# Kernel tuning notes

Hardware: AMD Instinct MI355X
Metric: run time of the kernel (lower is better)

Reference implementation:

```python
import jax, jax.numpy as jnp
import numpy as np

N_NODES = 50000
N_EDGES = 1600000
D_FEAT = 512
FILTERS = 256
NUM_CLASSES = 16


def setup_inputs() -> dict:
    key = jax.random.key(0)
    k = jax.random.split(key, 6)
    x = jax.random.normal(k[0], (N_NODES, D_FEAT), dtype=jnp.float32)
    W1 = jax.random.normal(k[1], (D_FEAT, FILTERS), dtype=jnp.float32) * (1.0 / np.sqrt(D_FEAT))
    W2 = jax.random.normal(k[2], (FILTERS, NUM_CLASSES), dtype=jnp.float32) * (1.0 / np.sqrt(FILTERS))
    edge_weight = jax.random.uniform(k[3], (N_EDGES,), dtype=jnp.float32)
    edge_src = jax.random.randint(k[4], (N_EDGES,), 0, N_NODES, dtype=jnp.int32)
    edge_dst = jax.random.randint(k[5], (N_EDGES,), 0, N_NODES, dtype=jnp.int32)
    return {"x": x, "W1": W1, "W2": W2, "edge_weight": edge_weight,
            "edge_src": edge_src, "edge_dst": edge_dst}


def _propagate(h, edge_src, edge_dst, edge_weight):
    # sparse A @ h: out[dst] += w * h[src]
    msgs = edge_weight[:, None] * h[edge_src]          # [E, F]
    return jax.ops.segment_sum(msgs, edge_dst, num_segments=N_NODES)


def reference(x, W1, W2, edge_weight, edge_src, edge_dst):
    # Dropout layers are identity at inference (training=False).
    # Layer 1: relu(A @ (X @ W1))
    h = jax.nn.relu(_propagate(x @ W1, edge_src, edge_dst, edge_weight))
    # Layer 2: softmax(A @ (H @ W2))
    logits = _propagate(h @ W2, edge_src, edge_dst, edge_weight)
    return jax.nn.softmax(logits, axis=-1)
```

## Files before the change

### kernel.cpp

```cpp
#include <hip/hip_runtime.h>

#define N_NODES 50000
#define N_EDGES 1600000
#define D_FEAT 512
#define FILTERS 256
#define NUM_CLASSES 16

typedef __bf16 bf16x8 __attribute__((ext_vector_type(8)));
typedef float f32x4 __attribute__((ext_vector_type(4)));
typedef _Float16 half4 __attribute__((ext_vector_type(4)));
typedef _Float16 f16x8 __attribute__((ext_vector_type(8)));

#define GLOAD_LDS16(g, l)                                                  \
  __builtin_amdgcn_global_load_lds(                                        \
      (const __attribute__((address_space(1))) unsigned int*)(g),          \
      (__attribute__((address_space(3))) unsigned int*)(l), 16, 0, 0)

__global__ __launch_bounds__(256) void split_w1_kernel(
    const float* __restrict__ W1, __bf16* __restrict__ Wth,
    __bf16* __restrict__ Wtl) {
  const int idx = blockIdx.x * 256 + threadIdx.x;
  const int k = idx >> 8;
  const int n = idx & 255;
  const float v = W1[idx];
  const __bf16 h = (__bf16)v;
  const __bf16 l = (__bf16)(v - (float)h);
  Wth[n * D_FEAT + k] = h;
  Wtl[n * D_FEAT + k] = l;
}

__global__ __launch_bounds__(256) void gemm1_mfma_kernel(
    const float* __restrict__ A, const __bf16* __restrict__ Bh,
    const __bf16* __restrict__ Bl, _Float16* __restrict__ C) {
  const int K = D_FEAT;
  __shared__ __bf16 sAh[128 * 32];
  __shared__ __bf16 sAl[128 * 32];
  __shared__ __bf16 sBh[128 * 32];
  __shared__ __bf16 sBl[128 * 32];

  const int tid = threadIdx.x;
  const int wave = tid >> 6;
  const int lane = tid & 63;
  const int wm = (wave >> 1) * 64;
  const int wn = (wave & 1) * 64;
  const int m0 = blockIdx.x * 128;
  const int n0 = blockIdx.y * 128;

  const int arow = tid >> 1;
  const int aks = (tid & 1) * 16;
  int am = m0 + arow;
  if (am >= N_NODES) am = N_NODES - 1;
  const float* aptr = A + (size_t)am * K + aks;

  const int lr = lane >> 2;
  const int lc = (lane & 3) * 8;
  const int fm = lane & 15;
  const int fq = lane >> 4;

  f32x4 acc[4][4] = {};

  for (int k0 = 0; k0 < K; k0 += 32) {
    const float4* ap = (const float4*)(aptr + k0);
    const float4 a0 = ap[0], a1 = ap[1], a2 = ap[2], a3 = ap[3];

    __syncthreads();

#pragma unroll
    for (int i = 0; i < 2; ++i) {
      const int row = wave * 32 + i * 16;
      GLOAD_LDS16(Bh + (size_t)(n0 + row + lr) * K + k0 + lc, sBh + row * 32);
      GLOAD_LDS16(Bl + (size_t)(n0 + row + lr) * K + k0 + lc, sBl + row * 32);
    }

    float va[16] = {a0.x, a0.y, a0.z, a0.w, a1.x, a1.y, a1.z, a1.w,
                    a2.x, a2.y, a2.z, a2.w, a3.x, a3.y, a3.z, a3.w};
    __bf16 hh[16], ll[16];
#pragma unroll
    for (int i = 0; i < 16; ++i) {
      const __bf16 h = (__bf16)va[i];
      hh[i] = h;
      ll[i] = (__bf16)(va[i] - (float)h);
    }
    *(bf16x8*)(sAh + arow * 32 + aks) = *(bf16x8*)&hh[0];
    *(bf16x8*)(sAh + arow * 32 + aks + 8) = *(bf16x8*)&hh[8];
    *(bf16x8*)(sAl + arow * 32 + aks) = *(bf16x8*)&ll[0];
    *(bf16x8*)(sAl + arow * 32 + aks + 8) = *(bf16x8*)&ll[8];

    __syncthreads();

    bf16x8 fah[4], fal[4], fbh[4], fbl[4];
#pragma unroll
    for (int t = 0; t < 4; ++t) {
      const int moff = (wm + t * 16 + fm) * 32 + fq * 8;
      fah[t] = *(const bf16x8*)(sAh + moff);
      fal[t] = *(const bf16x8*)(sAl + moff);
      const int noff = (wn + t * 16 + fm) * 32 + fq * 8;
      fbh[t] = *(const bf16x8*)(sBh + noff);
      fbl[t] = *(const bf16x8*)(sBl + noff);
    }
#pragma unroll
    for (int i = 0; i < 4; ++i)
#pragma unroll
      for (int j = 0; j < 4; ++j)
        acc[i][j] = __builtin_amdgcn_mfma_f32_16x16x32_bf16(fah[i], fbh[j],
                                                            acc[i][j], 0, 0, 0);
#pragma unroll
    for (int i = 0; i < 4; ++i)
#pragma unroll
      for (int j = 0; j < 4; ++j)
        acc[i][j] = __builtin_amdgcn_mfma_f32_16x16x32_bf16(fah[i], fbl[j],
                                                            acc[i][j], 0, 0, 0);
#pragma unroll
    for (int i = 0; i < 4; ++i)
#pragma unroll
      for (int j = 0; j < 4; ++j)
        acc[i][j] = __builtin_amdgcn_mfma_f32_16x16x32_bf16(fal[i], fbh[j],
                                                            acc[i][j], 0, 0, 0);
  }

#pragma unroll
  for (int ti = 0; ti < 4; ++ti) {
#pragma unroll
    for (int r = 0; r < 4; ++r) {
      const int m = m0 + wm + ti * 16 + fq * 4 + r;
      if (m < N_NODES) {
#pragma unroll
        for (int tj = 0; tj < 4; ++tj) {
          const int n = n0 + wn + tj * 16 + fm;
          C[(size_t)m * FILTERS + n] = (_Float16)acc[ti][tj][r];
        }
      }
    }
  }
}

__global__ __launch_bounds__(256) void hist_kernel(const int* __restrict__ edst,
                                                   int* __restrict__ deg) {
  const int e = blockIdx.x * 256 + threadIdx.x;
  if (e < N_EDGES) atomicAdd(&deg[edst[e]], 1);
}

#define SCAN_NB 196
__global__ __launch_bounds__(256) void scan_blocks_kernel(
    const int* __restrict__ deg, int* __restrict__ row_ptr,
    int* __restrict__ bsum) {
  __shared__ int s[256];
  const int i = blockIdx.x * 256 + threadIdx.x;
  const int v = (i < N_NODES) ? deg[i] : 0;
  s[threadIdx.x] = v;
  __syncthreads();
  for (int off = 1; off < 256; off <<= 1) {
    const int t = (threadIdx.x >= off) ? s[threadIdx.x - off] : 0;
    __syncthreads();
    s[threadIdx.x] += t;
    __syncthreads();
  }
  if (i < N_NODES) row_ptr[i] = s[threadIdx.x] - v;
  if (threadIdx.x == 255) bsum[blockIdx.x] = s[255];
}

__global__ __launch_bounds__(256) void scan_sums_kernel(int* __restrict__ bsum) {
  __shared__ int s[256];
  const int v = (threadIdx.x < SCAN_NB) ? bsum[threadIdx.x] : 0;
  s[threadIdx.x] = v;
  __syncthreads();
  for (int off = 1; off < 256; off <<= 1) {
    const int t = (threadIdx.x >= off) ? s[threadIdx.x - off] : 0;
    __syncthreads();
    s[threadIdx.x] += t;
    __syncthreads();
  }
  if (threadIdx.x < SCAN_NB) bsum[threadIdx.x] = s[threadIdx.x] - v;
}

__global__ __launch_bounds__(256) void scan_add_kernel(
    int* __restrict__ row_ptr, const int* __restrict__ bsum,
    int* __restrict__ cursor) {
  const int i = blockIdx.x * 256 + threadIdx.x;
  if (i < N_NODES) {
    const int r = row_ptr[i] + bsum[blockIdx.x];
    row_ptr[i] = r;
    cursor[i] = r;
  }
  if (i == 0) row_ptr[N_NODES] = N_EDGES;
}

__global__ __launch_bounds__(256) void fill_kernel(
    const int* __restrict__ esrc, const int* __restrict__ edst,
    const float* __restrict__ ew, int* __restrict__ cursor,
    int4* __restrict__ meta) {
  const int e = blockIdx.x * 256 + threadIdx.x;
  if (e >= N_EDGES) return;
  const int d = edst[e];
  const int pos = atomicAdd(&cursor[d], 1);
  meta[pos] = make_int4(esrc[e], __float_as_int(ew[e]), d, 0);
}

__global__ __launch_bounds__(256) void gather1_gemm2_kernel(
    const _Float16* __restrict__ xw1, const int* __restrict__ row_ptr,
    const int4* __restrict__ meta, const float* __restrict__ W2,
    _Float16* __restrict__ h2) {
  __shared__ float red[4][16][17];
  const int wave = threadIdx.x >> 6;
  const int lane = threadIdx.x & 63;
  const int node = blockIdx.x * 4 + wave;
  const int beg = row_ptr[node];
  const int end = row_ptr[node + 1];

  float acc[4] = {};
  const half4* __restrict__ xw1v = (const half4*)xw1;

  for (int c0 = beg; c0 < end; c0 += 64) {
    const int cnt = min(64, end - c0);
    const int4 mv = meta[c0 + ((lane < cnt) ? lane : 0)];

    for (int j = 0; j < cnt; j += 8) {
      int srcs[8];
      float ws[8];
#pragma unroll
      for (int u = 0; u < 8; ++u) {
        const int live = (j + u < cnt);
        const int l = live ? (j + u) : 0;
        srcs[u] = __builtin_amdgcn_readlane(mv.x, l);
        const int wb = __builtin_amdgcn_readlane(mv.y, l);
        ws[u] = live ? __int_as_float(wb) : 0.f;
      }
      half4 v[8];
#pragma unroll
      for (int u = 0; u < 8; ++u)
        v[u] = xw1v[(unsigned)srcs[u] * 64u + (unsigned)lane];
#pragma unroll
      for (int u = 0; u < 8; ++u)
#pragma unroll
        for (int i = 0; i < 4; ++i)
          acc[i] = fmaf(ws[u], (float)v[u][i], acc[i]);
    }
  }

  float r[4];
#pragma unroll
  for (int i = 0; i < 4; ++i) r[i] = fmaxf(acc[i], 0.f);

  float p[16] = {};
#pragma unroll
  for (int j = 0; j < 4; ++j) {
    const float4* wr = (const float4*)(W2 + (size_t)(lane * 4 + j) * NUM_CLASSES);
#pragma unroll
    for (int c4 = 0; c4 < 4; ++c4) {
      const float4 wv = wr[c4];
      p[c4 * 4 + 0] = fmaf(r[j], wv.x, p[c4 * 4 + 0]);
      p[c4 * 4 + 1] = fmaf(r[j], wv.y, p[c4 * 4 + 1]);
      p[c4 * 4 + 2] = fmaf(r[j], wv.z, p[c4 * 4 + 2]);
      p[c4 * 4 + 3] = fmaf(r[j], wv.w, p[c4 * 4 + 3]);
    }
  }

#pragma unroll
  for (int off = 32; off >= 16; off >>= 1)
#pragma unroll
    for (int i = 0; i < 16; ++i) p[i] += __shfl_xor(p[i], off, 64);

  if (lane < 16) {
#pragma unroll
    for (int i = 0; i < 16; ++i) red[wave][lane][i] = p[i];
  }
  if (lane < 16) {
    float sum = 0.f;
#pragma unroll
    for (int i = 0; i < 16; ++i) sum += red[wave][i][lane];
    h2[(size_t)node * NUM_CLASSES + lane] = (_Float16)sum;
  }
}

__global__ __launch_bounds__(256) void gather2_mfma_kernel(
    const _Float16* __restrict__ h2, const int* __restrict__ row_ptr,
    const int4* __restrict__ meta, float* __restrict__ out) {
  __shared__ _Float16 lds[4][16][72];
  const int wave = threadIdx.x >> 6;
  const int lane = threadIdx.x & 63;
  const int tile = blockIdx.x * 4 + wave;
  if (tile >= N_NODES / 16) return;
  const int t0 = tile * 16;
  const int beg = row_ptr[t0];
  const int end = row_ptr[t0 + 16];

  const int cls = lane & 15;
  const int kq = lane >> 4;
  const int erow = lane >> 1;
  const int part = lane & 1;

  f32x4 acc = {0.f, 0.f, 0.f, 0.f};
  _Float16* myl = &lds[wave][0][0];

  if (beg < end) {
    const int last = end - 1;
    int e = beg + lane;
    int4 m = meta[(e <= last) ? e : last];
    float wv = (e <= last) ? __int_as_float(m.y) : 0.f;

    for (int c0 = beg; c0 < end; c0 += 64) {
      int4 mn = m;
      float wn = 0.f;
      const int c1 = c0 + 64;
      if (c1 < end) {
        const int en = c1 + lane;
        mn = meta[(en <= last) ? en : last];
        wn = (en <= last) ? __int_as_float(mn.y) : 0.f;
      }

      const int se0 = __shfl(m.x, erow, 64);
      const int se1 = __shfl(m.x, 32 + erow, 64);
      const f16x8 r0 =
          *(const f16x8*)(h2 + (size_t)se0 * NUM_CLASSES + part * 8);
      const f16x8 r1 =
          *(const f16x8*)(h2 + (size_t)se1 * NUM_CLASSES + part * 8);

      f16x8 a0, a1;
#pragma unroll
      for (int j = 0; j < 8; ++j) {
        const int ei = kq * 8 + j;
        const int d0 = __shfl(m.z, ei, 64) - t0;
        const float w0 = __shfl(wv, ei, 64);
        a0[j] = (d0 == cls) ? (_Float16)w0 : (_Float16)0.f;
        const int d1 = __shfl(m.z, 32 + ei, 64) - t0;
        const float w1 = __shfl(wv, 32 + ei, 64);
        a1[j] = (d1 == cls) ? (_Float16)w1 : (_Float16)0.f;
      }

#pragma unroll
      for (int j = 0; j < 8; ++j) myl[(part * 8 + j) * 72 + erow] = r0[j];
#pragma unroll
      for (int j = 0; j < 8; ++j) myl[(part * 8 + j) * 72 + 32 + erow] = r1[j];

      const f16x8 b0 = *(const f16x8*)(myl + cls * 72 + kq * 8);
      const f16x8 b1 = *(const f16x8*)(myl + cls * 72 + 32 + kq * 8);

      acc = __builtin_amdgcn_mfma_f32_16x16x32_f16(a0, b0, acc, 0, 0, 0);
      acc = __builtin_amdgcn_mfma_f32_16x16x32_f16(a1, b1, acc, 0, 0, 0);

      m = mn;
      wv = wn;
    }
  }

#pragma unroll
  for (int r = 0; r < 4; ++r) {
    const float a = acc[r];
    float mx = a;
#pragma unroll
    for (int off = 8; off >= 1; off >>= 1)
      mx = fmaxf(mx, __shfl_xor(mx, off, 16));
    const float ex = __expf(a - mx);
    float sm = ex;
#pragma unroll
    for (int off = 8; off >= 1; off >>= 1) sm += __shfl_xor(sm, off, 16);
    out[(size_t)(t0 + kq * 4 + r) * NUM_CLASSES + cls] = ex / sm;
  }
}

extern "C" void kernel_launch(void* const* d_in, const int* in_sizes, int n_in,
                              void* d_out, int out_size, void* d_ws,
                              size_t ws_size, hipStream_t stream) {
  const float* x = (const float*)d_in[0];
  const float* W1 = (const float*)d_in[1];
  const float* W2 = (const float*)d_in[2];
  const float* ew = (const float*)d_in[3];
  const int* esrc = (const int*)d_in[4];
  const int* edst = (const int*)d_in[5];
  float* out = (float*)d_out;

  _Float16* xw1 = (_Float16*)d_ws;
  _Float16* h2 = xw1 + (size_t)N_NODES * FILTERS;
  int* row_ptr = (int*)(h2 + (size_t)N_NODES * NUM_CLASSES);
  int* cursor = row_ptr + (N_NODES + 1);
  int* deg = cursor + N_NODES;
  int4* meta = (int4*)(((uintptr_t)(deg + N_NODES) + 15) & ~(uintptr_t)15);
  __bf16* w1th = (__bf16*)(meta + N_EDGES);
  __bf16* w1tl = w1th + D_FEAT * FILTERS;
  int* bsum = (int*)(w1tl + D_FEAT * FILTERS);

  hipMemsetAsync(deg, 0, N_NODES * sizeof(int), stream);
  hist_kernel<<<(N_EDGES + 255) / 256, 256, 0, stream>>>(edst, deg);
  scan_blocks_kernel<<<SCAN_NB, 256, 0, stream>>>(deg, row_ptr, bsum);
  scan_sums_kernel<<<1, 256, 0, stream>>>(bsum);
  scan_add_kernel<<<SCAN_NB, 256, 0, stream>>>(row_ptr, bsum, cursor);
  fill_kernel<<<(N_EDGES + 255) / 256, 256, 0, stream>>>(esrc, edst, ew,
                                                         cursor, meta);

  split_w1_kernel<<<(D_FEAT * FILTERS) / 256, 256, 0, stream>>>(W1, w1th, w1tl);
  dim3 g1((N_NODES + 127) / 128, FILTERS / 128);
  gemm1_mfma_kernel<<<g1, 256, 0, stream>>>(x, w1th, w1tl, xw1);

  gather1_gemm2_kernel<<<N_NODES / 4, 256, 0, stream>>>(xw1, row_ptr, meta, W2,
                                                        h2);

  gather2_mfma_kernel<<<(N_NODES / 16 + 3) / 4, 256, 0, stream>>>(h2, row_ptr,
                                                                  meta, out);
}
```

Baseline: 564.1 us.

## Privatize degree histogram and fill cursors per XCD to avoid cross-die atomics

```diff
diff --git a/kernel.cpp b/kernel.cpp
--- a/kernel.cpp
+++ b/kernel.cpp
@@ -5,6 +5,7 @@
 #define D_FEAT 512
 #define FILTERS 256
 #define NUM_CLASSES 16
+#define NXCD 8
 
 typedef __bf16 bf16x8 __attribute__((ext_vector_type(8)));
 typedef float f32x4 __attribute__((ext_vector_type(4)));
@@ -29,6 +30,79 @@
   Wtl[n * D_FEAT + k] = l;
 }
 
+__global__ __launch_bounds__(256) void hist8_kernel(
+    const int* __restrict__ edst, int* __restrict__ deg8) {
+  const int e = blockIdx.x * 256 + threadIdx.x;
+  if (e >= N_EDGES) return;
+  const int x = blockIdx.x & (NXCD - 1);
+  atomicAdd(&deg8[x * N_NODES + edst[e]], 1);
+}
+
+#define SCAN_NB 196
+__global__ __launch_bounds__(256) void scan_blocks_kernel(
+    const int* __restrict__ deg8, int* __restrict__ row_ptr,
+    int* __restrict__ bsum) {
+  __shared__ int s[256];
+  const int i = blockIdx.x * 256 + threadIdx.x;
+  int v = 0;
+  if (i < N_NODES) {
+#pragma unroll
+    for (int x = 0; x < NXCD; ++x) v += deg8[x * N_NODES + i];
+  }
+  s[threadIdx.x] = v;
+  __syncthreads();
+  for (int off = 1; off < 256; off <<= 1) {
+    const int t = (threadIdx.x >= off) ? s[threadIdx.x - off] : 0;
+    __syncthreads();
+    s[threadIdx.x] += t;
+    __syncthreads();
+  }
+  if (i < N_NODES) row_ptr[i] = s[threadIdx.x] - v;
+  if (threadIdx.x == 255) bsum[blockIdx.x] = s[255];
+}
+
+__global__ __launch_bounds__(256) void scan_sums_kernel(int* __restrict__ bsum) {
+  __shared__ int s[256];
+  const int v = (threadIdx.x < SCAN_NB) ? bsum[threadIdx.x] : 0;
+  s[threadIdx.x] = v;
+  __syncthreads();
+  for (int off = 1; off < 256; off <<= 1) {
+    const int t = (threadIdx.x >= off) ? s[threadIdx.x - off] : 0;
+    __syncthreads();
+    s[threadIdx.x] += t;
+    __syncthreads();
+  }
+  if (threadIdx.x < SCAN_NB) bsum[threadIdx.x] = s[threadIdx.x] - v;
+}
+
+__global__ __launch_bounds__(256) void scan_add_cursor8_kernel(
+    int* __restrict__ row_ptr, const int* __restrict__ bsum,
+    const int* __restrict__ deg8, int* __restrict__ cursor8) {
+  const int i = blockIdx.x * 256 + threadIdx.x;
+  if (i < N_NODES) {
+    int run = row_ptr[i] + bsum[blockIdx.x];
+    row_ptr[i] = run;
+#pragma unroll
+    for (int x = 0; x < NXCD; ++x) {
+      cursor8[x * N_NODES + i] = run;
+      run += deg8[x * N_NODES + i];
+    }
+  }
+  if (i == 0) row_ptr[N_NODES] = N_EDGES;
+}
+
+__global__ __launch_bounds__(256) void fill8_kernel(
+    const int* __restrict__ esrc, const int* __restrict__ edst,
+    const float* __restrict__ ew, int* __restrict__ cursor8,
+    int4* __restrict__ meta) {
+  const int e = blockIdx.x * 256 + threadIdx.x;
+  if (e >= N_EDGES) return;
+  const int x = blockIdx.x & (NXCD - 1);
+  const int d = edst[e];
+  const int pos = atomicAdd(&cursor8[x * N_NODES + d], 1);
+  meta[pos] = make_int4(esrc[e], __float_as_int(ew[e]), d, 0);
+}
+
 __global__ __launch_bounds__(256) void gemm1_mfma_kernel(
     const float* __restrict__ A, const __bf16* __restrict__ Bh,
     const __bf16* __restrict__ Bl, _Float16* __restrict__ C) {
@@ -132,68 +206,6 @@
       }
     }
   }
-}
-
-__global__ __launch_bounds__(256) void hist_kernel(const int* __restrict__ edst,
-                                                   int* __restrict__ deg) {
-  const int e = blockIdx.x * 256 + threadIdx.x;
-  if (e < N_EDGES) atomicAdd(&deg[edst[e]], 1);
-}
-
-#define SCAN_NB 196
-__global__ __launch_bounds__(256) void scan_blocks_kernel(
-    const int* __restrict__ deg, int* __restrict__ row_ptr,
-    int* __restrict__ bsum) {
-  __shared__ int s[256];
-  const int i = blockIdx.x * 256 + threadIdx.x;
-  const int v = (i < N_NODES) ? deg[i] : 0;
-  s[threadIdx.x] = v;
-  __syncthreads();
-  for (int off = 1; off < 256; off <<= 1) {
-    const int t = (threadIdx.x >= off) ? s[threadIdx.x - off] : 0;
-    __syncthreads();
-    s[threadIdx.x] += t;
-    __syncthreads();
-  }
-  if (i < N_NODES) row_ptr[i] = s[threadIdx.x] - v;
-  if (threadIdx.x == 255) bsum[blockIdx.x] = s[255];
-}
-
-__global__ __launch_bounds__(256) void scan_sums_kernel(int* __restrict__ bsum) {
-  __shared__ int s[256];
-  const int v = (threadIdx.x < SCAN_NB) ? bsum[threadIdx.x] : 0;
-  s[threadIdx.x] = v;
-  __syncthreads();
-  for (int off = 1; off < 256; off <<= 1) {
-    const int t = (threadIdx.x >= off) ? s[threadIdx.x - off] : 0;
-    __syncthreads();
-    s[threadIdx.x] += t;
-    __syncthreads();
-  }
-  if (threadIdx.x < SCAN_NB) bsum[threadIdx.x] = s[threadIdx.x] - v;
-}
-
-__global__ __launch_bounds__(256) void scan_add_kernel(
-    int* __restrict__ row_ptr, const int* __restrict__ bsum,
-    int* __restrict__ cursor) {
-  const int i = blockIdx.x * 256 + threadIdx.x;
-  if (i < N_NODES) {
-    const int r = row_ptr[i] + bsum[blockIdx.x];
-    row_ptr[i] = r;
-    cursor[i] = r;
-  }
-  if (i == 0) row_ptr[N_NODES] = N_EDGES;
-}
-
-__global__ __launch_bounds__(256) void fill_kernel(
-    const int* __restrict__ esrc, const int* __restrict__ edst,
-    const float* __restrict__ ew, int* __restrict__ cursor,
-    int4* __restrict__ meta) {
-  const int e = blockIdx.x * 256 + threadIdx.x;
-  if (e >= N_EDGES) return;
-  const int d = edst[e];
-  const int pos = atomicAdd(&cursor[d], 1);
-  meta[pos] = make_int4(esrc[e], __float_as_int(ew[e]), d, 0);
 }
 
 __global__ __launch_bounds__(256) void gather1_gemm2_kernel(
@@ -372,20 +384,22 @@
   _Float16* xw1 = (_Float16*)d_ws;
   _Float16* h2 = xw1 + (size_t)N_NODES * FILTERS;
   int* row_ptr = (int*)(h2 + (size_t)N_NODES * NUM_CLASSES);
-  int* cursor = row_ptr + (N_NODES + 1);
-  int* deg = cursor + N_NODES;
-  int4* meta = (int4*)(((uintptr_t)(deg + N_NODES) + 15) & ~(uintptr_t)15);
+  int* deg8 = row_ptr + (N_NODES + 1);
+  int* cursor8 = deg8 + NXCD * N_NODES;
+  int4* meta = (int4*)(((uintptr_t)(cursor8 + NXCD * N_NODES) + 15) &
+                       ~(uintptr_t)15);
   __bf16* w1th = (__bf16*)(meta + N_EDGES);
   __bf16* w1tl = w1th + D_FEAT * FILTERS;
   int* bsum = (int*)(w1tl + D_FEAT * FILTERS);
 
-  hipMemsetAsync(deg, 0, N_NODES * sizeof(int), stream);
-  hist_kernel<<<(N_EDGES + 255) / 256, 256, 0, stream>>>(edst, deg);
-  scan_blocks_kernel<<<SCAN_NB, 256, 0, stream>>>(deg, row_ptr, bsum);
+  hipMemsetAsync(deg8, 0, NXCD * N_NODES * sizeof(int), stream);
+  hist8_kernel<<<(N_EDGES + 255) / 256, 256, 0, stream>>>(edst, deg8);
+  scan_blocks_kernel<<<SCAN_NB, 256, 0, stream>>>(deg8, row_ptr, bsum);
   scan_sums_kernel<<<1, 256, 0, stream>>>(bsum);
-  scan_add_kernel<<<SCAN_NB, 256, 0, stream>>>(row_ptr, bsum, cursor);
-  fill_kernel<<<(N_EDGES + 255) / 256, 256, 0, stream>>>(esrc, edst, ew,
-                                                         cursor, meta);
+  scan_add_cursor8_kernel<<<SCAN_NB, 256, 0, stream>>>(row_ptr, bsum, deg8,
+                                                       cursor8);
+  fill8_kernel<<<(N_EDGES + 255) / 256, 256, 0, stream>>>(esrc, edst, ew,
+                                                          cursor8, meta);
 
   split_w1_kernel<<<(D_FEAT * FILTERS) / 256, 256, 0, stream>>>(W1, w1th, w1tl);
   dim3 g1((N_NODES + 127) / 128, FILTERS / 128);
```

After: 555.8 us. No clear change (-1.5%).
